# Kernel optimization log

Measured on AMD Instinct MI355X. Metric: run time of the kernel, lower is better.

The kernel has to match this reference:

```python
import jax, jax.numpy as jnp
import numpy as np

B, N, E, V, D, H = 16, 4096, 524288, 4, 64, 128
MLP_IN = H + 3 + 2  # node feats + conditioning coords + two temperature scalars
SRC_T, TGT_T = 300.0, 600.0
SCALE_RANGE = 0.5


def _w(k, shape):
    return (jax.random.normal(k, shape, jnp.float32) / np.sqrt(shape[0])).astype(jnp.float32)


def setup_inputs() -> dict:
    key = jax.random.key(0)
    ks = jax.random.split(key, 32)
    inp = {
        "coordinates": jax.random.normal(ks[0], (B, N, 3), jnp.float32),
        "atom_types": jax.random.randint(ks[1], (B, N), 0, V, jnp.int32),
        "adj_list": jax.random.randint(ks[2], (E, 2), 0, N, jnp.int32),
        "edge_batch_idx": jax.random.randint(ks[3], (E,), 0, B, jnp.int32),
        "masked_elements": jnp.zeros((B, N), bool),
        # message-passing GNN params
        "embed": jax.random.normal(ks[4], (V, D), jnp.float32),
        "W_in": _w(ks[5], (D + 3, H)), "b_in": jnp.zeros(H, jnp.float32),
        "W_msg0": _w(ks[6], (2 * H, H)), "b_msg0": jnp.zeros(H, jnp.float32),
        "W_upd0": _w(ks[7], (2 * H, H)), "b_upd0": jnp.zeros(H, jnp.float32),
        "W_msg1": _w(ks[8], (2 * H, H)), "b_msg1": jnp.zeros(H, jnp.float32),
        "W_upd1": _w(ks[9], (2 * H, H)), "b_upd1": jnp.zeros(H, jnp.float32),
        "W_out": _w(ks[10], (H, H)), "b_out": jnp.zeros(H, jnp.float32),
        # scale MLP (random small weights instead of zero init so output is non-trivial)
        "Ws0": _w(ks[11], (MLP_IN, H)), "bs0": jnp.zeros(H, jnp.float32),
        "Ws1": _w(ks[12], (H, H)), "bs1": jnp.zeros(H, jnp.float32),
        "Ws2": _w(ks[13], (H, H // 2)), "bs2": jnp.zeros(H // 2, jnp.float32),
        "Ws3": _w(ks[14], (H // 2, 3)) * 0.1, "bs3": jnp.zeros(3, jnp.float32),
        # shift MLP
        "Wt0": _w(ks[15], (MLP_IN, H)), "bt0": jnp.zeros(H, jnp.float32),
        "Wt1": _w(ks[16], (H, H)), "bt1": jnp.zeros(H, jnp.float32),
        "Wt2": _w(ks[17], (H, H // 2)), "bt2": jnp.zeros(H // 2, jnp.float32),
        "Wt3": _w(ks[18], (H // 2, 3)) * 0.1, "bt3": jnp.zeros(3, jnp.float32),
    }
    return inp


def _mlp(x, layers):
    for Wl, bl in layers[:-1]:
        x = jax.nn.relu(x @ Wl + bl)
    Wl, bl = layers[-1]
    return x @ Wl + bl


def reference(coordinates, atom_types, adj_list, edge_batch_idx, masked_elements,
              embed, W_in, b_in, W_msg0, b_msg0, W_upd0, b_upd0,
              W_msg1, b_msg1, W_upd1, b_upd1, W_out, b_out,
              Ws0, bs0, Ws1, bs1, Ws2, bs2, Ws3, bs3,
              Wt0, bt0, Wt1, bt1, Wt2, bt2, Wt3, bt3):
    Bn, Nn, _ = coordinates.shape
    valid = ~masked_elements                              # [B,N]
    vf = valid[..., None].astype(coordinates.dtype)
    # ---- message passing GNN ----
    h = jnp.concatenate([embed[atom_types], coordinates], -1)  # [B,N,D+3]
    h = jax.nn.relu(h @ W_in + b_in) * vf
    hf = h.reshape(Bn * Nn, -1)
    src = edge_batch_idx * Nn + adj_list[:, 0]
    dst = edge_batch_idx * Nn + adj_list[:, 1]
    for Wm, bm, Wu, bu in ((W_msg0, b_msg0, W_upd0, b_upd0),
                           (W_msg1, b_msg1, W_upd1, b_upd1)):
        m = jax.nn.relu(jnp.concatenate([hf[src], hf[dst]], -1) @ Wm + bm)  # [E,H]
        agg = jax.ops.segment_sum(m, dst, num_segments=Bn * Nn)             # [B*N,H]
        hf = jax.nn.relu(jnp.concatenate([hf, agg], -1) @ Wu + bu)
    node_feats = (hf @ W_out + b_out).reshape(Bn, Nn, -1) * vf              # [B,N,H]
    # ---- coupling transform (phase=0: atoms with type>0 are transformed) ----
    coupling = (atom_types > 0) & valid                  # [B,N]
    cond = coordinates * (~coupling)[..., None].astype(coordinates.dtype)
    temps = jnp.broadcast_to(jnp.asarray([SRC_T, TGT_T], coordinates.dtype), (Bn, Nn, 2))
    x = jnp.concatenate([node_feats, cond, temps], -1)   # [B,N,H+5]
    raw_scales = _mlp(x, [(Ws0, bs0), (Ws1, bs1), (Ws2, bs2), (Ws3, bs3)])
    shifts = _mlp(x, [(Wt0, bt0), (Wt1, bt1), (Wt2, bt2), (Wt3, bt3)])
    m3 = coupling[..., None].astype(coordinates.dtype)   # [B,N,1]
    log_scales = jnp.tanh(raw_scales) * SCALE_RANGE * m3 * vf
    shifts = shifts * m3
    log_det = log_scales.sum((1, 2))                     # [B]
    out = jnp.exp(log_scales) * coordinates + shifts
    out = jnp.where(coupling[..., None], out, coordinates)
    return out, log_det
```

## Files before the change

kernel.cpp:

```cpp
#include <hip/hip_runtime.h>

#define NB    16
#define NN    4096
#define NNODE (NB*NN)
#define NE    524288

typedef __attribute__((ext_vector_type(8))) short bf16x8_t;
typedef __attribute__((ext_vector_type(4))) float f32x4_t;

__device__ __forceinline__ unsigned short f2bf(float f) {
    union { float f; unsigned u; } v; v.f = f;
    return (unsigned short)((v.u + 0x7FFFu + ((v.u >> 16) & 1u)) >> 16);
}
__device__ __forceinline__ float bf2f(unsigned short h) {
    union { unsigned u; float f; } v; v.u = ((unsigned)h) << 16;
    return v.f;
}

__device__ __forceinline__ void gld16(const void* g, void* l) {
    __builtin_amdgcn_global_load_lds(
        (const __attribute__((address_space(1))) unsigned int*)g,
        (__attribute__((address_space(3))) unsigned int*)l, 16, 0, 0);
}

__global__ void deg_k(const int* __restrict__ adj, const int* __restrict__ ebi, int* __restrict__ deg)
{
    int e = blockIdx.x * 256 + threadIdx.x;
    atomicAdd(&deg[ebi[e] * NN + adj[2 * e + 1]], 1);
}

__global__ void scan_k(const int* __restrict__ deg, int* __restrict__ offs)
{
    __shared__ int sums[1024];
    int t = threadIdx.x;
    int base = t * 64;
    int s = 0;
    for (int i = 0; i < 64; ++i) s += deg[base + i];
    sums[t] = s;
    __syncthreads();
    for (int off = 1; off < 1024; off <<= 1) {
        int add = (t >= off) ? sums[t - off] : 0;
        __syncthreads();
        sums[t] += add;
        __syncthreads();
    }
    int run = (t > 0) ? sums[t - 1] : 0;
    for (int i = 0; i < 64; ++i) { offs[base + i] = run; run += deg[base + i]; }
    if (t == 1023) offs[NNODE] = run;
}

__global__ void scat_k(const int* __restrict__ adj, const int* __restrict__ ebi,
                       const int* __restrict__ offs, int* __restrict__ cur, int* __restrict__ esrc)
{
    int e = blockIdx.x * 256 + threadIdx.x;
    int bb = ebi[e];
    int d = bb * NN + adj[2 * e + 1];
    int s = bb * NN + adj[2 * e + 0];
    esrc[offs[d] + atomicAdd(&cur[d], 1)] = s;
}

__global__ void prep_k(const float* __restrict__ Wm0, const float* __restrict__ Wm1,
                       const float* __restrict__ Wu0, const float* __restrict__ Wu1,
                       const float* __restrict__ Wout,
                       const float* __restrict__ Ws0, const float* __restrict__ Wt0,
                       const float* __restrict__ Ws1, const float* __restrict__ Wt1,
                       const float* __restrict__ Ws2, const float* __restrict__ Wt2,
                       const float* __restrict__ bs0, const float* __restrict__ bt0,
                       const float* __restrict__ bs1, const float* __restrict__ bt1,
                       const float* __restrict__ bs2, const float* __restrict__ bt2,
                       const float* __restrict__ bm0, const float* __restrict__ bm1,
                       unsigned short* __restrict__ Btm0, unsigned short* __restrict__ Btm1,
                       unsigned short* __restrict__ Btu0, unsigned short* __restrict__ Btu1,
                       unsigned short* __restrict__ WoutP,
                       unsigned short* __restrict__ Bt0cat, unsigned short* __restrict__ Bt1cat,
                       unsigned short* __restrict__ Bt2cat,
                       float* __restrict__ b0cat, float* __restrict__ b1cat,
                       float* __restrict__ b2cat,
                       float* __restrict__ bm0cat, float* __restrict__ bm1cat,
                       int* __restrict__ deg, int* __restrict__ cur)
{
    int bid = blockIdx.x, tx = threadIdx.x;
    if (bid < 256) {
        const float* W = bid < 128 ? Wm0 : Wm1;
        unsigned short* Bt = bid < 128 ? Btm0 : Btm1;
        int idx = (bid & 127) * 256 + tx;
        int n = idx >> 7, k = idx & 127;
        float v = (n < 128) ? W[k * 128 + n] : W[(128 + k) * 128 + (n - 128)];
        Bt[n * 128 + k] = f2bf(v);
    } else if (bid < 512) {
        const float* W = bid < 384 ? Wu0 : Wu1;
        unsigned short* Bt = bid < 384 ? Btu0 : Btu1;
        int idx = ((bid - 256) & 127) * 256 + tx;
        int n = idx >> 8, k = idx & 255;
        Bt[n * 256 + k] = f2bf(W[k * 128 + n]);
    } else if (bid < 576) {
        int idx = (bid - 512) * 256 + tx;
        int n = idx >> 7, k = idx & 127;
        WoutP[n * 128 + k] = f2bf(Wout[k * 128 + n]);
    } else if (bid < 768) {
        int idx = (bid - 576) * 256 + tx;
        int n = idx / 192, kk = idx % 192;
        const float* W = n < 128 ? Ws0 : Wt0;
        int nn = n & 127;
        Bt0cat[n * 192 + kk] = f2bf(kk < 133 ? W[kk * 128 + nn] : 0.f);
    } else if (bid < 896) {
        int idx = (bid - 768) * 256 + tx;
        int n = idx >> 7, k = idx & 127;
        const float* W = n < 128 ? Ws1 : Wt1;
        Bt1cat[n * 128 + k] = f2bf(W[k * 128 + (n & 127)]);
    } else if (bid < 1024) {
        int idx = (bid - 896) * 256 + tx;
        int n = idx >> 7, k = idx & 127;
        const float* W = n < 128 ? Ws2 : Wt2;
        int nn = n & 127;
        Bt2cat[n * 128 + k] = f2bf(nn < 64 ? W[k * 64 + nn] : 0.f);
    } else if (bid == 1024) {
        b0cat[tx] = (tx < 128) ? bs0[tx] : bt0[tx - 128];
    } else if (bid == 1025) {
        b1cat[tx] = (tx < 128) ? bs1[tx] : bt1[tx - 128];
    } else if (bid == 1026) {
        int nn = tx & 127;
        b2cat[tx] = (nn < 64) ? ((tx < 128) ? bs2[nn] : bt2[nn]) : 0.f;
    } else if (bid == 1027) {
        bm0cat[tx] = (tx < 128) ? 0.f : bm0[tx - 128];
    } else if (bid == 1028) {
        bm1cat[tx] = (tx < 128) ? 0.f : bm1[tx - 128];
    } else {
        int idx = (bid - 1029) * 256 + tx;
        int4 z = {0, 0, 0, 0};
        if (idx < 16384) ((int4*)deg)[idx] = z;
        else             ((int4*)cur)[idx - 16384] = z;
    }
}

__device__ __forceinline__ void gather_agg(char* aggLds, const unsigned short* __restrict__ P12,
    const int* __restrict__ offs, const int* __restrict__ esrc, size_t row0, int tx)
{
#pragma unroll
    for (int it = 0; it < 4; ++it) {
        int r = it * 16 + (tx >> 4);
        int l = tx & 15;
        size_t node = row0 + r;
        int beg = offs[node], end = offs[node + 1];
        float p2c[8], ac[8];
        {
            uint4 w = *(const uint4*)(P12 + node * 256 + 128 + 8 * l);
            unsigned ww[4] = {w.x, w.y, w.z, w.w};
#pragma unroll
            for (int j = 0; j < 4; ++j) {
                p2c[2*j]   = bf2f((unsigned short)(ww[j] & 0xFFFF));
                p2c[2*j+1] = bf2f((unsigned short)(ww[j] >> 16));
            }
        }
#pragma unroll
        for (int j = 0; j < 8; ++j) ac[j] = 0.f;
        auto accum = [&](uint4 v) {
            unsigned ww[4] = {v.x, v.y, v.z, v.w};
#pragma unroll
            for (int j = 0; j < 4; ++j) {
                ac[2*j]   += fmaxf(bf2f((unsigned short)(ww[j] & 0xFFFF)) + p2c[2*j],   0.f);
                ac[2*j+1] += fmaxf(bf2f((unsigned short)(ww[j] >> 16))    + p2c[2*j+1], 0.f);
            }
        };
        int i = beg;
        for (; i + 3 < end; i += 4) {
            int s0 = esrc[i], s1 = esrc[i+1], s2 = esrc[i+2], s3 = esrc[i+3];
            uint4 v0 = *(const uint4*)(P12 + (size_t)s0 * 256 + 8 * l);
            uint4 v1 = *(const uint4*)(P12 + (size_t)s1 * 256 + 8 * l);
            uint4 v2 = *(const uint4*)(P12 + (size_t)s2 * 256 + 8 * l);
            uint4 v3 = *(const uint4*)(P12 + (size_t)s3 * 256 + 8 * l);
            accum(v0); accum(v1); accum(v2); accum(v3);
        }
        for (; i < end; ++i) {
            uint4 v0 = *(const uint4*)(P12 + (size_t)esrc[i] * 256 + 8 * l);
            accum(v0);
        }
        uint4 o;
        o.x = (unsigned)f2bf(ac[0]) | ((unsigned)f2bf(ac[1]) << 16);
        o.y = (unsigned)f2bf(ac[2]) | ((unsigned)f2bf(ac[3]) << 16);
        o.z = (unsigned)f2bf(ac[4]) | ((unsigned)f2bf(ac[5]) << 16);
        o.w = (unsigned)f2bf(ac[6]) | ((unsigned)f2bf(ac[7]) << 16);
        int cb = l * 16;
        *(uint4*)(aggLds + r * 256 + (cb & ~127) + ((cb & 127) ^ ((r & 7) << 4))) = o;
    }
}

__device__ __forceinline__ void msg_phase(const char* act, char* Bs,
    const unsigned short* __restrict__ Bt, const float* __restrict__ bias,
    unsigned short* __restrict__ P12, size_t row0, int tx)
{
    const int wid = tx >> 6, l = tx & 63;
    const int wr = wid >> 1, wc = wid & 1;
    const int rsel = l & 15, kq = l >> 4;
    const int rg = l >> 4, cc = l & 15;
#pragma unroll
    for (int nh = 0; nh < 2; ++nh) {
        f32x4_t acc[2][4];
#pragma unroll
        for (int i = 0; i < 2; ++i)
#pragma unroll
            for (int j = 0; j < 4; ++j) { f32x4_t z = {0.f,0.f,0.f,0.f}; acc[i][j] = z; }
#pragma unroll
        for (int kc = 0; kc < 128; kc += 64) {
            __syncthreads();
#pragma unroll
            for (int p = 0; p < 4; ++p) {
                int idx = tx + p * 256;
                int n = idx >> 3, kg = idx & 7;
                int kgs = kg ^ (n & 7);
                gld16(Bt + (size_t)(nh * 128 + n) * 128 + kc + kgs * 8, Bs + idx * 16);
            }
            __syncthreads();
#pragma unroll
            for (int ks = 0; ks < 2; ++ks) {
                bf16x8_t af[2], bv[4];
#pragma unroll
                for (int fm = 0; fm < 2; ++fm) {
                    int r = wr * 32 + fm * 16 + rsel;
                    af[fm] = *(const bf16x8_t*)(act + r * 256 + kc * 2 + ((ks * 64 + kq * 16) ^ ((r & 7) << 4)));
                }
#pragma unroll
                for (int fn = 0; fn < 4; ++fn) {
                    int n = wc * 64 + fn * 16 + rsel;
                    bv[fn] = *(const bf16x8_t*)(Bs + n * 128 + ((ks * 64 + kq * 16) ^ ((n & 7) << 4)));
                }
#pragma unroll
                for (int fm = 0; fm < 2; ++fm)
#pragma unroll
                    for (int fn = 0; fn < 4; ++fn)
                        acc[fm][fn] = __builtin_amdgcn_mfma_f32_16x16x32_bf16(af[fm], bv[fn], acc[fm][fn], 0, 0, 0);
            }
        }
        __syncthreads();
#pragma unroll
        for (int fm = 0; fm < 2; ++fm)
#pragma unroll
            for (int rr = 0; rr < 4; ++rr) {
                int row = wr * 32 + fm * 16 + rg * 4 + rr;
#pragma unroll
                for (int fn = 0; fn < 4; ++fn) {
                    int col = wc * 64 + fn * 16 + cc;
                    float v = acc[fm][fn][rr] + bias[nh * 128 + col];
                    int cb = col * 2;
                    *(unsigned short*)(Bs + row * 256 + (cb & ~127) + ((cb & 127) ^ ((row & 7) << 4))) = f2bf(v);
                }
            }
        __syncthreads();
#pragma unroll
        for (int p = 0; p < 4; ++p) {
            int idx = tx + p * 256;
            int row = idx >> 4, g = idx & 15;
            int pb = g * 16;
            uint4 v = *(const uint4*)(Bs + row * 256 + (pb & ~127) + ((pb & 127) ^ ((row & 7) << 4)));
            *(uint4*)(P12 + (row0 + row) * 256 + nh * 128 + g * 8) = v;
        }
    }
}

__launch_bounds__(256, 4)
__global__ void fused_im_k(const int* __restrict__ types, const float* __restrict__ coords,
                           const unsigned char* __restrict__ maskb,
                           const float* __restrict__ embed, const float* __restrict__ W_in,
                           const float* __restrict__ b_in,
                           const unsigned short* __restrict__ Btm, const float* __restrict__ bmcat,
                           unsigned short* __restrict__ hf, unsigned short* __restrict__ P12)
{
    __shared__ __align__(16) char act[16384];
    __shared__ __align__(16) char Bs[16384];
    const int tx = threadIdx.x;
    const int tile = ((blockIdx.x & 7) * (gridDim.x >> 3)) + (blockIdx.x >> 3);
    const size_t row0 = (size_t)tile * 64;

    float* wf = (float*)Bs;
    float* xs = (float*)(Bs + 4096);
#pragma unroll
    for (int p = 0; p < 4; ++p) {
        int idx = tx + p * 256;
        int k = idx >> 7, c = idx & 127;
        wf[idx] = (k < 7) ? W_in[k * 128 + c] : b_in[c];
    }
    if (tx < 64) {
        size_t node = row0 + tx;
        int tp = types[node];
#pragma unroll
        for (int j = 0; j < 4; ++j) xs[tx * 8 + j] = embed[(size_t)tp * 4 + j];
#pragma unroll
        for (int j = 0; j < 3; ++j) xs[tx * 8 + 4 + j] = coords[node * 3 + j];
    }
    __syncthreads();
    {
        int row = tx >> 2, c0 = (tx & 3) * 32;
        float x0 = xs[row*8+0], x1 = xs[row*8+1], x2 = xs[row*8+2], x3 = xs[row*8+3];
        float x4 = xs[row*8+4], x5 = xs[row*8+5], x6 = xs[row*8+6];
        bool msk = maskb[row0 + row];
        int swz = (row & 7) << 4;
#pragma unroll
        for (int c = 0; c < 32; ++c) {
            int col = c0 + c;
            float a = wf[7*128+col] + x0*wf[col] + x1*wf[128+col] + x2*wf[256+col]
                    + x3*wf[384+col] + x4*wf[512+col] + x5*wf[640+col] + x6*wf[768+col];
            a = msk ? 0.f : fmaxf(a, 0.f);
            int cb = col * 2;
            *(unsigned short*)(act + row * 256 + (cb & ~127) + ((cb & 127) ^ swz)) = f2bf(a);
        }
    }
    __syncthreads();
#pragma unroll
    for (int p = 0; p < 4; ++p) {
        int idx = tx + p * 256;
        int row = idx >> 4, g = idx & 15;
        int pb = g * 16;
        uint4 v = *(const uint4*)(act + row * 256 + (pb & ~127) + ((pb & 127) ^ ((row & 7) << 4)));
        *(uint4*)(hf + (row0 + row) * 128 + g * 8) = v;
    }
    msg_phase(act, Bs, Btm, bmcat, P12, row0, tx);
}

__launch_bounds__(256, 4)
__global__ void fused_um_k(const unsigned short* __restrict__ hfin,
                           const unsigned short* __restrict__ P12in,
                           const int* __restrict__ offs, const int* __restrict__ esrc,
                           const unsigned short* __restrict__ Btu, const float* __restrict__ bu,
                           const unsigned short* __restrict__ Btm, const float* __restrict__ bmcat,
                           unsigned short* __restrict__ hfout, unsigned short* __restrict__ P12)
{
    __shared__ __align__(16) char act[16384];
    __shared__ __align__(16) char Bs[16384];
    const int tx = threadIdx.x;
    const int wid = tx >> 6, l = tx & 63;
    const int wr = wid >> 1, wc = wid & 1;
    const int rsel = l & 15, kq = l >> 4, rg = l >> 4, cc = l & 15;
    const int tile = ((blockIdx.x & 7) * (gridDim.x >> 3)) + (blockIdx.x >> 3);
    const size_t row0 = (size_t)tile * 64;

    gather_agg(act, P12in, offs, esrc, row0, tx);

    f32x4_t acc[2][4];
#pragma unroll
    for (int i = 0; i < 2; ++i)
#pragma unroll
        for (int j = 0; j < 4; ++j) { f32x4_t z = {0.f,0.f,0.f,0.f}; acc[i][j] = z; }
#pragma unroll
    for (int kc = 0; kc < 256; kc += 64) {
        int kloc = kc & 127;
        __syncthreads();
#pragma unroll
        for (int p = 0; p < 4; ++p) {
            int idx = tx + p * 256;
            int n = idx >> 3, kg = idx & 7;
            int kgs = kg ^ (n & 7);
            gld16(Btu + (size_t)n * 256 + kc + kgs * 8, Bs + idx * 16);
        }
        __syncthreads();
#pragma unroll
        for (int ks = 0; ks < 2; ++ks) {
            bf16x8_t af[2], bv[4];
#pragma unroll
            for (int fm = 0; fm < 2; ++fm) {
                int r = wr * 32 + fm * 16 + rsel;
                if (kc < 128) {
                    af[fm] = *(const bf16x8_t*)(hfin + (row0 + r) * 128 + kloc + ks * 32 + kq * 8);
                } else {
                    af[fm] = *(const bf16x8_t*)(act + r * 256 + kloc * 2 + ((ks * 64 + kq * 16) ^ ((r & 7) << 4)));
                }
            }
#pragma unroll
            for (int fn = 0; fn < 4; ++fn) {
                int n = wc * 64 + fn * 16 + rsel;
                bv[fn] = *(const bf16x8_t*)(Bs + n * 128 + ((ks * 64 + kq * 16) ^ ((n & 7) << 4)));
            }
#pragma unroll
            for (int fm = 0; fm < 2; ++fm)
#pragma unroll
                for (int fn = 0; fn < 4; ++fn)
                    acc[fm][fn] = __builtin_amdgcn_mfma_f32_16x16x32_bf16(af[fm], bv[fn], acc[fm][fn], 0, 0, 0);
        }
    }
    __syncthreads();
#pragma unroll
    for (int fm = 0; fm < 2; ++fm)
#pragma unroll
        for (int rr = 0; rr < 4; ++rr) {
            int row = wr * 32 + fm * 16 + rg * 4 + rr;
#pragma unroll
            for (int fn = 0; fn < 4; ++fn) {
                int col = wc * 64 + fn * 16 + cc;
                float v = fmaxf(acc[fm][fn][rr] + bu[col], 0.f);
                int cb = col * 2;
                *(unsigned short*)(act + row * 256 + (cb & ~127) + ((cb & 127) ^ ((row & 7) << 4))) = f2bf(v);
            }
        }
    __syncthreads();
#pragma unroll
    for (int p = 0; p < 4; ++p) {
        int idx = tx + p * 256;
        int row = idx >> 4, g = idx & 15;
        int pb = g * 16;
        uint4 v = *(const uint4*)(act + row * 256 + (pb & ~127) + ((pb & 127) ^ ((row & 7) << 4)));
        *(uint4*)(hfout + (row0 + row) * 128 + g * 8) = v;
    }
    msg_phase(act, Bs, Btm, bmcat, P12, row0, tx);
}

__launch_bounds__(256, 2)
__global__ void fused_ut_k(const unsigned short* __restrict__ hfin,
                           const unsigned short* __restrict__ P12in,
                           const int* __restrict__ offs, const int* __restrict__ esrc,
                           const unsigned short* __restrict__ Btu, const float* __restrict__ bu,
                           const unsigned short* __restrict__ WoutP, const float* __restrict__ bOut,
                           const unsigned short* __restrict__ Bt0, const float* __restrict__ b0,
                           const unsigned short* __restrict__ Bt1, const float* __restrict__ b1,
                           const unsigned short* __restrict__ Bt2, const float* __restrict__ b2,
                           const float* __restrict__ Ws3, const float* __restrict__ bs3,
                           const float* __restrict__ Wt3, const float* __restrict__ bt3,
                           const float* __restrict__ coords, const int* __restrict__ types,
                           const unsigned char* __restrict__ maskb,
                           float* __restrict__ outc, float* __restrict__ partial)
{
    __shared__ __align__(16) char act[32768];
    __shared__ __align__(16) char hfn[16384];
    __shared__ __align__(16) char Bs[32768];
    const int tx = threadIdx.x;
    const int wid = tx >> 6, l = tx & 63;
    const int rsel = l & 15, kq = l >> 4, rg = l >> 4, cc = l & 15;
    const int tile = ((blockIdx.x & 7) * (gridDim.x >> 3)) + (blockIdx.x >> 3);
    const size_t row0 = (size_t)tile * 64;
    const int wr = wid >> 1, wc = wid & 1;

    gather_agg(act, P12in, offs, esrc, row0, tx);

    {
        f32x4_t acc[2][4];
#pragma unroll
        for (int i = 0; i < 2; ++i)
#pragma unroll
            for (int j = 0; j < 4; ++j) { f32x4_t z = {0.f,0.f,0.f,0.f}; acc[i][j] = z; }
#pragma unroll
        for (int kc = 0; kc < 256; kc += 64) {
            int kloc = kc & 127;
            __syncthreads();
#pragma unroll
            for (int p = 0; p < 4; ++p) {
                int idx = tx + p * 256;
                int n = idx >> 3, kg = idx & 7;
                int kgs = kg ^ (n & 7);
                gld16(Btu + (size_t)n * 256 + kc + kgs * 8, Bs + idx * 16);
            }
            __syncthreads();
#pragma unroll
            for (int ks = 0; ks < 2; ++ks) {
                bf16x8_t af[2], bv[4];
#pragma unroll
                for (int fm = 0; fm < 2; ++fm) {
                    int r = wr * 32 + fm * 16 + rsel;
                    if (kc < 128) {
                        af[fm] = *(const bf16x8_t*)(hfin + (row0 + r) * 128 + kloc + ks * 32 + kq * 8);
                    } else {
                        af[fm] = *(const bf16x8_t*)(act + r * 256 + kloc * 2 + ((ks * 64 + kq * 16) ^ ((r & 7) << 4)));
                    }
                }
#pragma unroll
                for (int fn = 0; fn < 4; ++fn) {
                    int n = wc * 64 + fn * 16 + rsel;
                    bv[fn] = *(const bf16x8_t*)(Bs + n * 128 + ((ks * 64 + kq * 16) ^ ((n & 7) << 4)));
                }
#pragma unroll
                for (int fm = 0; fm < 2; ++fm)
#pragma unroll
                    for (int fn = 0; fn < 4; ++fn)
                        acc[fm][fn] = __builtin_amdgcn_mfma_f32_16x16x32_bf16(af[fm], bv[fn], acc[fm][fn], 0, 0, 0);
            }
        }
#pragma unroll
        for (int fm = 0; fm < 2; ++fm)
#pragma unroll
            for (int rr = 0; rr < 4; ++rr) {
                int row = wr * 32 + fm * 16 + rg * 4 + rr;
#pragma unroll
                for (int fn = 0; fn < 4; ++fn) {
                    int col = wc * 64 + fn * 16 + cc;
                    float v = fmaxf(acc[fm][fn][rr] + bu[col], 0.f);
                    int cb = col * 2;
                    *(unsigned short*)(hfn + row * 256 + (cb & ~127) + ((cb & 127) ^ ((row & 7) << 4))) = f2bf(v);
                }
            }
    }
    __syncthreads();

    {
        f32x4_t acc[2][4];
#pragma unroll
        for (int i = 0; i < 2; ++i)
#pragma unroll
            for (int j = 0; j < 4; ++j) { f32x4_t z = {0.f,0.f,0.f,0.f}; acc[i][j] = z; }
#pragma unroll
        for (int kc = 0; kc < 128; kc += 64) {
            __syncthreads();
#pragma unroll
            for (int p = 0; p < 4; ++p) {
                int idx = tx + p * 256;
                int n = idx >> 3, kg = idx & 7;
                int kgs = kg ^ (n & 7);
                gld16(WoutP + (size_t)n * 128 + kc + kgs * 8, Bs + idx * 16);
            }
            __syncthreads();
#pragma unroll
            for (int ks = 0; ks < 2; ++ks) {
                bf16x8_t af[2], bv[4];
#pragma unroll
                for (int fm = 0; fm < 2; ++fm) {
                    int r = wr * 32 + fm * 16 + rsel;
                    af[fm] = *(const bf16x8_t*)(hfn + r * 256 + kc * 2 + ((ks * 64 + kq * 16) ^ ((r & 7) << 4)));
                }
#pragma unroll
                for (int fn = 0; fn < 4; ++fn) {
                    int n = wc * 64 + fn * 16 + rsel;
                    bv[fn] = *(const bf16x8_t*)(Bs + n * 128 + ((ks * 64 + kq * 16) ^ ((n & 7) << 4)));
                }
#pragma unroll
                for (int fm = 0; fm < 2; ++fm)
#pragma unroll
                    for (int fn = 0; fn < 4; ++fn)
                        acc[fm][fn] = __builtin_amdgcn_mfma_f32_16x16x32_bf16(af[fm], bv[fn], acc[fm][fn], 0, 0, 0);
            }
        }
        __syncthreads();
#pragma unroll
        for (int fm = 0; fm < 2; ++fm)
#pragma unroll
            for (int rr = 0; rr < 4; ++rr) {
                int row = wr * 32 + fm * 16 + rg * 4 + rr;
                bool zero = maskb[row0 + row];
#pragma unroll
                for (int fn = 0; fn < 4; ++fn) {
                    int col = wc * 64 + fn * 16 + cc;
                    float v = acc[fm][fn][rr] + bOut[col];
                    if (zero) v = 0.f;
                    int cb = col * 2;
                    *(unsigned short*)(act + row * 512 + (cb & ~127) + ((cb & 127) ^ ((row & 7) << 4))) = f2bf(v);
                }
            }
    }
#pragma unroll
    for (int p = 0; p < 16; ++p) {
        int idx = tx + p * 256;
        int row = idx >> 6, ci = idx & 63;
        int col = 128 + ci;
        size_t node = row0 + row;
        bool coup = (types[node] > 0) && !maskb[node];
        float v;
        if (ci < 3)       v = coup ? 0.f : coords[node * 3 + ci];
        else if (ci == 3) v = 300.f;
        else if (ci == 4) v = 600.f;
        else              v = 0.f;
        int cb = col * 2;
        *(unsigned short*)(act + row * 512 + (cb & ~127) + ((cb & 127) ^ ((row & 7) << 4))) = f2bf(v);
    }
    __syncthreads();

#pragma unroll
    for (int layer = 0; layer < 3; ++layer) {
        const unsigned short* Bt = layer == 0 ? Bt0 : (layer == 1 ? Bt1 : Bt2);
        const float* bb = layer == 0 ? b0 : (layer == 1 ? b1 : b2);
        const int ldbt = layer == 0 ? 192 : 128;
        const int Ktot = layer == 0 ? 192 : 128;
        const int kbase = (layer == 0) ? 0 : (wc ? 256 : 0);
        f32x4_t acc[2][8];
#pragma unroll
        for (int i = 0; i < 2; ++i)
#pragma unroll
            for (int j = 0; j < 8; ++j) { f32x4_t z = {0.f,0.f,0.f,0.f}; acc[i][j] = z; }
        for (int kc = 0; kc < Ktot; kc += 64) {
            __syncthreads();
#pragma unroll
            for (int p = 0; p < 8; ++p) {
                int idx = tx + p * 256;
                int n = idx >> 3, kg = idx & 7;
                int kgs = kg ^ (n & 7);
                gld16(Bt + (size_t)n * ldbt + kc + kgs * 8, Bs + idx * 16);
            }
            __syncthreads();
#pragma unroll
            for (int ks = 0; ks < 2; ++ks) {
                bf16x8_t af[2], bv[8];
#pragma unroll
                for (int fm = 0; fm < 2; ++fm) {
                    int r = wr * 32 + fm * 16 + rsel;
                    af[fm] = *(const bf16x8_t*)(act + r * 512 + kbase + kc * 2 + ((ks * 64 + kq * 16) ^ ((r & 7) << 4)));
                }
#pragma unroll
                for (int fn = 0; fn < 8; ++fn) {
                    int n = wc * 128 + fn * 16 + rsel;
                    bv[fn] = *(const bf16x8_t*)(Bs + n * 128 + ((ks * 64 + kq * 16) ^ ((n & 7) << 4)));
                }
#pragma unroll
                for (int fm = 0; fm < 2; ++fm)
#pragma unroll
                    for (int fn = 0; fn < 8; ++fn)
                        acc[fm][fn] = __builtin_amdgcn_mfma_f32_16x16x32_bf16(af[fm], bv[fn], acc[fm][fn], 0, 0, 0);
            }
        }
        __syncthreads();
#pragma unroll
        for (int fm = 0; fm < 2; ++fm)
#pragma unroll
            for (int rr = 0; rr < 4; ++rr) {
                int row = wr * 32 + fm * 16 + rg * 4 + rr;
#pragma unroll
                for (int fn = 0; fn < 8; ++fn) {
                    int col = wc * 128 + fn * 16 + cc;
                    float v = fmaxf(acc[fm][fn][rr] + bb[col], 0.f);
                    int cb = col * 2;
                    *(unsigned short*)(act + row * 512 + (cb & ~127) + ((cb & 127) ^ ((row & 7) << 4))) = f2bf(v);
                }
            }
        __syncthreads();
    }

    float* W3f = (float*)hfn;
    float* red = (float*)(hfn + 2048);
    for (int i = tx; i < 384; i += 256)
        W3f[i] = (i < 192) ? Ws3[i] : Wt3[i - 192];
    __syncthreads();
    {
        int row = tx >> 2, sub = tx & 3;
        int swz = (row & 7) << 4;
        float rs0 = 0.f, rs1 = 0.f, rs2 = 0.f, sh0 = 0.f, sh1 = 0.f, sh2 = 0.f;
#pragma unroll
        for (int kk = 0; kk < 16; ++kk) {
            int k = sub * 16 + kk;
            float av = bf2f(*(const unsigned short*)(act + row * 512 + ((k * 2) ^ swz)));
            float bv = bf2f(*(const unsigned short*)(act + row * 512 + 256 + ((k * 2) ^ swz)));
            rs0 += av * W3f[k * 3 + 0]; rs1 += av * W3f[k * 3 + 1]; rs2 += av * W3f[k * 3 + 2];
            sh0 += bv * W3f[192 + k * 3 + 0]; sh1 += bv * W3f[192 + k * 3 + 1]; sh2 += bv * W3f[192 + k * 3 + 2];
        }
        rs0 += __shfl_xor(rs0, 1); rs0 += __shfl_xor(rs0, 2);
        rs1 += __shfl_xor(rs1, 1); rs1 += __shfl_xor(rs1, 2);
        rs2 += __shfl_xor(rs2, 1); rs2 += __shfl_xor(rs2, 2);
        sh0 += __shfl_xor(sh0, 1); sh0 += __shfl_xor(sh0, 2);
        sh1 += __shfl_xor(sh1, 1); sh1 += __shfl_xor(sh1, 2);
        sh2 += __shfl_xor(sh2, 1); sh2 += __shfl_xor(sh2, 2);
        if (sub == 0) {
            size_t node = row0 + row;
            bool coup = (types[node] > 0) && !maskb[node];
            float c0 = coords[node * 3 + 0], c1 = coords[node * 3 + 1], c2 = coords[node * 3 + 2];
            float ls0 = 0.f, ls1 = 0.f, ls2 = 0.f, o0 = c0, o1 = c1, o2 = c2;
            if (coup) {
                ls0 = tanhf(rs0 + bs3[0]) * 0.5f;
                ls1 = tanhf(rs1 + bs3[1]) * 0.5f;
                ls2 = tanhf(rs2 + bs3[2]) * 0.5f;
                o0 = expf(ls0) * c0 + sh0 + bt3[0];
                o1 = expf(ls1) * c1 + sh1 + bt3[1];
                o2 = expf(ls2) * c2 + sh2 + bt3[2];
            }
            outc[node * 3 + 0] = o0;
            outc[node * 3 + 1] = o1;
            outc[node * 3 + 2] = o2;
            red[row] = ls0 + ls1 + ls2;
        }
    }
    __syncthreads();
    for (int s = 32; s > 0; s >>= 1) {
        if (tx < s) red[tx] += red[tx + s];
        __syncthreads();
    }
    if (tx == 0) partial[tile] = red[0];
}

__global__ void red_k(const float* __restrict__ partial, float* __restrict__ ldet)
{
    __shared__ float s[1024];
    int t = threadIdx.x;
#pragma unroll
    for (int p = 0; p < 4; ++p) s[t + p * 256] = partial[t + p * 256];
    __syncthreads();
    if (t < 16) {
        float v = 0.f;
        for (int i = 0; i < 64; ++i) v += s[t * 64 + i];
        ldet[t] = v;
    }
}

extern "C" void kernel_launch(void* const* d_in, const int* in_sizes, int n_in,
                              void* d_out, int out_size, void* d_ws, size_t ws_size,
                              hipStream_t stream)
{
    (void)in_sizes; (void)n_in; (void)out_size; (void)ws_size;
    const float* coords = (const float*)d_in[0];
    const int*   types  = (const int*)d_in[1];
    const int*   adj    = (const int*)d_in[2];
    const int*   ebi    = (const int*)d_in[3];
    const unsigned char* maskb = (const unsigned char*)d_in[4];
    const float* embed  = (const float*)d_in[5];
    const float* W_in   = (const float*)d_in[6];
    const float* b_in   = (const float*)d_in[7];
    const float* W_msg[2] = {(const float*)d_in[8],  (const float*)d_in[12]};
    const float* b_msg[2] = {(const float*)d_in[9],  (const float*)d_in[13]};
    const float* W_upd[2] = {(const float*)d_in[10], (const float*)d_in[14]};
    const float* b_upd[2] = {(const float*)d_in[11], (const float*)d_in[15]};
    const float* W_out = (const float*)d_in[16]; const float* b_out = (const float*)d_in[17];
    const float* Ws0 = (const float*)d_in[18]; const float* bs0 = (const float*)d_in[19];
    const float* Ws1 = (const float*)d_in[20]; const float* bs1 = (const float*)d_in[21];
    const float* Ws2 = (const float*)d_in[22]; const float* bs2 = (const float*)d_in[23];
    const float* Ws3 = (const float*)d_in[24]; const float* bs3 = (const float*)d_in[25];
    const float* Wt0 = (const float*)d_in[26]; const float* bt0 = (const float*)d_in[27];
    const float* Wt1 = (const float*)d_in[28]; const float* bt1 = (const float*)d_in[29];
    const float* Wt2 = (const float*)d_in[30]; const float* bt2 = (const float*)d_in[31];
    const float* Wt3 = (const float*)d_in[32]; const float* bt3 = (const float*)d_in[33];

    char* ws = (char*)d_ws;
    size_t off = 0;
    auto alloc = [&](size_t bytes) { void* p = ws + off; off += (bytes + 255) & ~(size_t)255; return p; };
    unsigned short* hf   = (unsigned short*)alloc((size_t)NNODE * 128 * 2);
    unsigned short* P12  = (unsigned short*)alloc((size_t)NNODE * 256 * 2);
    int*   deg  = (int*)alloc((size_t)NNODE * 4);
    int*   offs = (int*)alloc((size_t)(NNODE + 1) * 4);
    int*   cur  = (int*)alloc((size_t)NNODE * 4);
    int*   esrc = (int*)alloc((size_t)NE * 4);
    unsigned short* Btm0 = (unsigned short*)alloc(256 * 128 * 2);
    unsigned short* Btm1 = (unsigned short*)alloc(256 * 128 * 2);
    unsigned short* Btu0 = (unsigned short*)alloc(128 * 256 * 2);
    unsigned short* Btu1 = (unsigned short*)alloc(128 * 256 * 2);
    unsigned short* WoutP  = (unsigned short*)alloc(128 * 128 * 2);
    unsigned short* Bt0cat = (unsigned short*)alloc(256 * 192 * 2);
    unsigned short* Bt1cat = (unsigned short*)alloc(256 * 128 * 2);
    unsigned short* Bt2cat = (unsigned short*)alloc(256 * 128 * 2);
    float* b0cat  = (float*)alloc(256 * 4);
    float* b1cat  = (float*)alloc(256 * 4);
    float* b2cat  = (float*)alloc(256 * 4);
    float* bm0cat = (float*)alloc(256 * 4);
    float* bm1cat = (float*)alloc(256 * 4);
    float* partial = (float*)alloc(1024 * 4);

    prep_k<<<1157, 256, 0, stream>>>(W_msg[0], W_msg[1], W_upd[0], W_upd[1], W_out,
                                     Ws0, Wt0, Ws1, Wt1, Ws2, Wt2,
                                     bs0, bt0, bs1, bt1, bs2, bt2, b_msg[0], b_msg[1],
                                     Btm0, Btm1, Btu0, Btu1, WoutP,
                                     Bt0cat, Bt1cat, Bt2cat,
                                     b0cat, b1cat, b2cat, bm0cat, bm1cat, deg, cur);
    deg_k<<<NE / 256, 256, 0, stream>>>(adj, ebi, deg);
    scan_k<<<1, 1024, 0, stream>>>(deg, offs);
    scat_k<<<NE / 256, 256, 0, stream>>>(adj, ebi, offs, cur, esrc);

    fused_im_k<<<1024, 256, 0, stream>>>(types, coords, maskb, embed, W_in, b_in,
                                         Btm0, bm0cat, hf, P12);
    fused_um_k<<<1024, 256, 0, stream>>>(hf, P12, offs, esrc, Btu0, b_upd[0],
                                         Btm1, bm1cat, hf, P12);
    float* outc = (float*)d_out;
    fused_ut_k<<<1024, 256, 0, stream>>>(hf, P12, offs, esrc, Btu1, b_upd[1], WoutP, b_out,
                                         Bt0cat, b0cat, Bt1cat, b1cat, Bt2cat, b2cat,
                                         Ws3, bs3, Wt3, bt3,
                                         coords, types, maskb, outc, partial);
    red_k<<<1, 256, 0, stream>>>(partial, outc + (size_t)NNODE * 3);
}
```

Before: 236.4 us.

## Use 512 threads per block in final fused kernel with inlined gather

Measured after the change: 224.1 us. 1.05x faster.

```diff
diff --git a/kernel.cpp b/kernel.cpp
--- a/kernel.cpp
+++ b/kernel.cpp
@@ -402,7 +402,7 @@
     msg_phase(act, Bs, Btm, bmcat, P12, row0, tx);
 }
 
-__launch_bounds__(256, 2)
+__launch_bounds__(512, 2)
 __global__ void fused_ut_k(const unsigned short* __restrict__ hfin,
                            const unsigned short* __restrict__ P12in,
                            const int* __restrict__ offs, const int* __restrict__ esrc,
@@ -425,23 +425,69 @@
     const int rsel = l & 15, kq = l >> 4, rg = l >> 4, cc = l & 15;
     const int tile = ((blockIdx.x & 7) * (gridDim.x >> 3)) + (blockIdx.x >> 3);
     const size_t row0 = (size_t)tile * 64;
-    const int wr = wid >> 1, wc = wid & 1;
-
-    gather_agg(act, P12in, offs, esrc, row0, tx);
+    const int wr = wid >> 2, wc4 = wid & 3;
+
+#pragma unroll
+    for (int it = 0; it < 2; ++it) {
+        int r = it * 32 + (tx >> 4);
+        int ll = tx & 15;
+        size_t node = row0 + r;
+        int beg = offs[node], end = offs[node + 1];
+        float p2c[8], ac[8];
+        {
+            uint4 w = *(const uint4*)(P12in + node * 256 + 128 + 8 * ll);
+            unsigned ww[4] = {w.x, w.y, w.z, w.w};
+#pragma unroll
+            for (int j = 0; j < 4; ++j) {
+                p2c[2*j]   = bf2f((unsigned short)(ww[j] & 0xFFFF));
+                p2c[2*j+1] = bf2f((unsigned short)(ww[j] >> 16));
+            }
+        }
+#pragma unroll
+        for (int j = 0; j < 8; ++j) ac[j] = 0.f;
+        auto accum = [&](uint4 v) {
+            unsigned ww[4] = {v.x, v.y, v.z, v.w};
+#pragma unroll
+            for (int j = 0; j < 4; ++j) {
+                ac[2*j]   += fmaxf(bf2f((unsigned short)(ww[j] & 0xFFFF)) + p2c[2*j],   0.f);
+                ac[2*j+1] += fmaxf(bf2f((unsigned short)(ww[j] >> 16))    + p2c[2*j+1], 0.f);
+            }
+        };
+        int i = beg;
+        for (; i + 3 < end; i += 4) {
+            int s0 = esrc[i], s1 = esrc[i+1], s2 = esrc[i+2], s3 = esrc[i+3];
+            uint4 v0 = *(const uint4*)(P12in + (size_t)s0 * 256 + 8 * ll);
+            uint4 v1 = *(const uint4*)(P12in + (size_t)s1 * 256 + 8 * ll);
+            uint4 v2 = *(const uint4*)(P12in + (size_t)s2 * 256 + 8 * ll);
+            uint4 v3 = *(const uint4*)(P12in + (size_t)s3 * 256 + 8 * ll);
+            accum(v0); accum(v1); accum(v2); accum(v3);
+        }
+        for (; i < end; ++i) {
+            uint4 v0 = *(const uint4*)(P12in + (size_t)esrc[i] * 256 + 8 * ll);
+            accum(v0);
+        }
+        uint4 o;
+        o.x = (unsigned)f2bf(ac[0]) | ((unsigned)f2bf(ac[1]) << 16);
+        o.y = (unsigned)f2bf(ac[2]) | ((unsigned)f2bf(ac[3]) << 16);
+        o.z = (unsigned)f2bf(ac[4]) | ((unsigned)f2bf(ac[5]) << 16);
+        o.w = (unsigned)f2bf(ac[6]) | ((unsigned)f2bf(ac[7]) << 16);
+        int cb = ll * 16;
+        *(uint4*)(act + r * 256 + (cb & ~127) + ((cb & 127) ^ ((r & 7) << 4))) = o;
+    }
 
     {
-        f32x4_t acc[2][4];
+        f32x4_t acc[2][2];
 #pragma unroll
         for (int i = 0; i < 2; ++i)
 #pragma unroll
-            for (int j = 0; j < 4; ++j) { f32x4_t z = {0.f,0.f,0.f,0.f}; acc[i][j] = z; }
+            for (int j = 0; j < 2; ++j) { f32x4_t z = {0.f,0.f,0.f,0.f}; acc[i][j] = z; }
 #pragma unroll
         for (int kc = 0; kc < 256; kc += 64) {
             int kloc = kc & 127;
             __syncthreads();
 #pragma unroll
-            for (int p = 0; p < 4; ++p) {
-                int idx = tx + p * 256;
+            for (int p = 0; p < 2; ++p) {
+                int idx = tx + p * 512;
                 int n = idx >> 3, kg = idx & 7;
                 int kgs = kg ^ (n & 7);
                 gld16(Btu + (size_t)n * 256 + kc + kgs * 8, Bs + idx * 16);
@@ -449,7 +495,7 @@
             __syncthreads();
 #pragma unroll
             for (int ks = 0; ks < 2; ++ks) {
-                bf16x8_t af[2], bv[4];
+                bf16x8_t af[2], bv[2];
 #pragma unroll
                 for (int fm = 0; fm < 2; ++fm) {
                     int r = wr * 32 + fm * 16 + rsel;
@@ -460,14 +506,14 @@
                     }
                 }
 #pragma unroll
-                for (int fn = 0; fn < 4; ++fn) {
-                    int n = wc * 64 + fn * 16 + rsel;
+                for (int fn = 0; fn < 2; ++fn) {
+                    int n = wc4 * 32 + fn * 16 + rsel;
                     bv[fn] = *(const bf16x8_t*)(Bs + n * 128 + ((ks * 64 + kq * 16) ^ ((n & 7) << 4)));
                 }
 #pragma unroll
                 for (int fm = 0; fm < 2; ++fm)
 #pragma unroll
-                    for (int fn = 0; fn < 4; ++fn)
+                    for (int fn = 0; fn < 2; ++fn)
                         acc[fm][fn] = __builtin_amdgcn_mfma_f32_16x16x32_bf16(af[fm], bv[fn], acc[fm][fn], 0, 0, 0);
             }
         }
@@ -477,8 +523,8 @@
             for (int rr = 0; rr < 4; ++rr) {
                 int row = wr * 32 + fm * 16 + rg * 4 + rr;
 #pragma unroll
-                for (int fn = 0; fn < 4; ++fn) {
-                    int col = wc * 64 + fn * 16 + cc;
+                for (int fn = 0; fn < 2; ++fn) {
+                    int col = wc4 * 32 + fn * 16 + cc;
                     float v = fmaxf(acc[fm][fn][rr] + bu[col], 0.f);
                     int cb = col * 2;
                     *(unsigned short*)(hfn + row * 256 + (cb & ~127) + ((cb & 127) ^ ((row & 7) << 4))) = f2bf(v);
@@ -488,17 +534,17 @@
     __syncthreads();
 
     {
-        f32x4_t acc[2][4];
+        f32x4_t acc[2][2];
 #pragma unroll
         for (int i = 0; i < 2; ++i)
 #pragma unroll
-            for (int j = 0; j < 4; ++j) { f32x4_t z = {0.f,0.f,0.f,0.f}; acc[i][j] = z; }
+            for (int j = 0; j < 2; ++j) { f32x4_t z = {0.f,0.f,0.f,0.f}; acc[i][j] = z; }
 #pragma unroll
         for (int kc = 0; kc < 128; kc += 64) {
             __syncthreads();
 #pragma unroll
-            for (int p = 0; p < 4; ++p) {
-                int idx = tx + p * 256;
+            for (int p = 0; p < 2; ++p) {
+                int idx = tx + p * 512;
                 int n = idx >> 3, kg = idx & 7;
                 int kgs = kg ^ (n & 7);
                 gld16(WoutP + (size_t)n * 128 + kc + kgs * 8, Bs + idx * 16);
@@ -506,21 +552,21 @@
             __syncthreads();
 #pragma unroll
             for (int ks = 0; ks < 2; ++ks) {
-                bf16x8_t af[2], bv[4];
+                bf16x8_t af[2], bv[2];
 #pragma unroll
                 for (int fm = 0; fm < 2; ++fm) {
                     int r = wr * 32 + fm * 16 + rsel;
                     af[fm] = *(const bf16x8_t*)(hfn + r * 256 + kc * 2 + ((ks * 64 + kq * 16) ^ ((r & 7) << 4)));
                 }
 #pragma unroll
-                for (int fn = 0; fn < 4; ++fn) {
-                    int n = wc * 64 + fn * 16 + rsel;
+                for (int fn = 0; fn < 2; ++fn) {
+                    int n = wc4 * 32 + fn * 16 + rsel;
                     bv[fn] = *(const bf16x8_t*)(Bs + n * 128 + ((ks * 64 + kq * 16) ^ ((n & 7) << 4)));
                 }
 #pragma unroll
                 for (int fm = 0; fm < 2; ++fm)
 #pragma unroll
-                    for (int fn = 0; fn < 4; ++fn)
+                    for (int fn = 0; fn < 2; ++fn)
                         acc[fm][fn] = __builtin_amdgcn_mfma_f32_16x16x32_bf16(af[fm], bv[fn], acc[fm][fn], 0, 0, 0);
             }
         }
@@ -532,8 +578,8 @@
                 int row = wr * 32 + fm * 16 + rg * 4 + rr;
                 bool zero = maskb[row0 + row];
 #pragma unroll
-                for (int fn = 0; fn < 4; ++fn) {
-                    int col = wc * 64 + fn * 16 + cc;
+                for (int fn = 0; fn < 2; ++fn) {
+                    int col = wc4 * 32 + fn * 16 + cc;
                     float v = acc[fm][fn][rr] + bOut[col];
                     if (zero) v = 0.f;
                     int cb = col * 2;
@@ -542,8 +588,8 @@
             }
     }
 #pragma unroll
-    for (int p = 0; p < 16; ++p) {
-        int idx = tx + p * 256;
+    for (int p = 0; p < 8; ++p) {
+        int idx = tx + p * 512;
         int row = idx >> 6, ci = idx & 63;
         int col = 128 + ci;
         size_t node = row0 + row;
@@ -564,17 +610,17 @@
         const float* bb = layer == 0 ? b0 : (layer == 1 ? b1 : b2);
         const int ldbt = layer == 0 ? 192 : 128;
         const int Ktot = layer == 0 ? 192 : 128;
-        const int kbase = (layer == 0) ? 0 : (wc ? 256 : 0);
-        f32x4_t acc[2][8];
+        const int kbase = (layer == 0) ? 0 : ((wc4 >= 2) ? 256 : 0);
+        f32x4_t acc[2][4];
 #pragma unroll
         for (int i = 0; i < 2; ++i)
 #pragma unroll
-            for (int j = 0; j < 8; ++j) { f32x4_t z = {0.f,0.f,0.f,0.f}; acc[i][j] = z; }
+            for (int j = 0; j < 4; ++j) { f32x4_t z = {0.f,0.f,0.f,0.f}; acc[i][j] = z; }
         for (int kc = 0; kc < Ktot; kc += 64) {
             __syncthreads();
 #pragma unroll
-            for (int p = 0; p < 8; ++p) {
-                int idx = tx + p * 256;
+            for (int p = 0; p < 4; ++p) {
+                int idx = tx + p * 512;
                 int n = idx >> 3, kg = idx & 7;
                 int kgs = kg ^ (n & 7);
                 gld16(Bt + (size_t)n * ldbt + kc + kgs * 8, Bs + idx * 16);
@@ -582,21 +628,21 @@
             __syncthreads();
 #pragma unroll
             for (int ks = 0; ks < 2; ++ks) {
-                bf16x8_t af[2], bv[8];
+                bf16x8_t af[2], bv[4];
 #pragma unroll
                 for (int fm = 0; fm < 2; ++fm) {
                     int r = wr * 32 + fm * 16 + rsel;
                     af[fm] = *(const bf16x8_t*)(act + r * 512 + kbase + kc * 2 + ((ks * 64 + kq * 16) ^ ((r & 7) << 4)));
                 }
 #pragma unroll
-                for (int fn = 0; fn < 8; ++fn) {
-                    int n = wc * 128 + fn * 16 + rsel;
+                for (int fn = 0; fn < 4; ++fn) {
+                    int n = wc4 * 64 + fn * 16 + rsel;
                     bv[fn] = *(const bf16x8_t*)(Bs + n * 128 + ((ks * 64 + kq * 16) ^ ((n & 7) << 4)));
                 }
 #pragma unroll
                 for (int fm = 0; fm < 2; ++fm)
 #pragma unroll
-                    for (int fn = 0; fn < 8; ++fn)
+                    for (int fn = 0; fn < 4; ++fn)
                         acc[fm][fn] = __builtin_amdgcn_mfma_f32_16x16x32_bf16(af[fm], bv[fn], acc[fm][fn], 0, 0, 0);
             }
         }
@@ -607,8 +653,8 @@
             for (int rr = 0; rr < 4; ++rr) {
                 int row = wr * 32 + fm * 16 + rg * 4 + rr;
 #pragma unroll
-                for (int fn = 0; fn < 8; ++fn) {
-                    int col = wc * 128 + fn * 16 + cc;
+                for (int fn = 0; fn < 4; ++fn) {
+                    int col = wc4 * 64 + fn * 16 + cc;
                     float v = fmaxf(acc[fm][fn][rr] + bb[col], 0.f);
                     int cb = col * 2;
                     *(unsigned short*)(act + row * 512 + (cb & ~127) + ((cb & 127) ^ ((row & 7) << 4))) = f2bf(v);
@@ -619,27 +665,27 @@
 
     float* W3f = (float*)hfn;
     float* red = (float*)(hfn + 2048);
-    for (int i = tx; i < 384; i += 256)
+    for (int i = tx; i < 384; i += 512)
         W3f[i] = (i < 192) ? Ws3[i] : Wt3[i - 192];
     __syncthreads();
     {
-        int row = tx >> 2, sub = tx & 3;
+        int row = tx >> 3, sub = tx & 7;
         int swz = (row & 7) << 4;
         float rs0 = 0.f, rs1 = 0.f, rs2 = 0.f, sh0 = 0.f, sh1 = 0.f, sh2 = 0.f;
 #pragma unroll
-        for (int kk = 0; kk < 16; ++kk) {
-            int k = sub * 16 + kk;
+        for (int kk = 0; kk < 8; ++kk) {
+            int k = sub * 8 + kk;
             float av = bf2f(*(const unsigned short*)(act + row * 512 + ((k * 2) ^ swz)));
             float bv = bf2f(*(const unsigned short*)(act + row * 512 + 256 + ((k * 2) ^ swz)));
             rs0 += av * W3f[k * 3 + 0]; rs1 += av * W3f[k * 3 + 1]; rs2 += av * W3f[k * 3 + 2];
             sh0 += bv * W3f[192 + k * 3 + 0]; sh1 += bv * W3f[192 + k * 3 + 1]; sh2 += bv * W3f[192 + k * 3 + 2];
         }
-        rs0 += __shfl_xor(rs0, 1); rs0 += __shfl_xor(rs0, 2);
-        rs1 += __shfl_xor(rs1, 1); rs1 += __shfl_xor(rs1, 2);
-        rs2 += __shfl_xor(rs2, 1); rs2 += __shfl_xor(rs2, 2);
-        sh0 += __shfl_xor(sh0, 1); sh0 += __shfl_xor(sh0, 2);
-        sh1 += __shfl_xor(sh1, 1); sh1 += __shfl_xor(sh1, 2);
-        sh2 += __shfl_xor(sh2, 1); sh2 += __shfl_xor(sh2, 2);
+        rs0 += __shfl_xor(rs0, 1); rs0 += __shfl_xor(rs0, 2); rs0 += __shfl_xor(rs0, 4);
+        rs1 += __shfl_xor(rs1, 1); rs1 += __shfl_xor(rs1, 2); rs1 += __shfl_xor(rs1, 4);
+        rs2 += __shfl_xor(rs2, 1); rs2 += __shfl_xor(rs2, 2); rs2 += __shfl_xor(rs2, 4);
+        sh0 += __shfl_xor(sh0, 1); sh0 += __shfl_xor(sh0, 2); sh0 += __shfl_xor(sh0, 4);
+        sh1 += __shfl_xor(sh1, 1); sh1 += __shfl_xor(sh1, 2); sh1 += __shfl_xor(sh1, 4);
+        sh2 += __shfl_xor(sh2, 1); sh2 += __shfl_xor(sh2, 2); sh2 += __shfl_xor(sh2, 4);
         if (sub == 0) {
             size_t node = row0 + row;
             bool coup = (types[node] > 0) && !maskb[node];
@@ -747,7 +793,7 @@
     fused_um_k<<<1024, 256, 0, stream>>>(hf, P12, offs, esrc, Btu0, b_upd[0],
                                          Btm1, bm1cat, hf, P12);
     float* outc = (float*)d_out;
-    fused_ut_k<<<1024, 256, 0, stream>>>(hf, P12, offs, esrc, Btu1, b_upd[1], WoutP, b_out,
+    fused_ut_k<<<1024, 512, 0, stream>>>(hf, P12, offs, esrc, Btu1, b_upd[1], WoutP, b_out,
                                          Bt0cat, b0cat, Bt1cat, b1cat, Bt2cat, b2cat,
                                          Ws3, bs3, Wt3, bt3,
                                          coords, types, maskb, outc, partial);
```
